# Kernel optimization log

Hardware: AMD Instinct MI355X
Metric: run time of the kernel (lower is better)

## Reference

```python
import jax, jax.numpy as jnp
import numpy as np

N_NODES = 100000
N_EDGES = 1600000
D_IN = 128
D_OUT = 128


def setup_inputs() -> dict:
    key = jax.random.key(0)
    k1, k2, k3, k4 = jax.random.split(key, 4)
    feat = jax.random.normal(k1, (N_NODES, D_IN), dtype=jnp.float32)
    W1 = jax.random.normal(k2, (D_OUT, D_IN), dtype=jnp.float32) * (1.0 / np.sqrt(D_IN))
    src = jax.random.randint(k3, (N_EDGES,), 0, N_NODES, dtype=jnp.int32)
    # ensure every dst node has at least one in-edge (no empty segments, like a
    # DGL graph without isolated destination nodes)
    dst_rand = jax.random.randint(k4, (N_EDGES - N_NODES,), 0, N_NODES, dtype=jnp.int32)
    dst = jnp.concatenate([jnp.arange(N_NODES, dtype=jnp.int32), dst_rand])
    return {"feat": feat, "W1": W1, "src": src, "dst": dst}


def reference(feat, W1, src, dst):
    # nn.Linear(bias=False): h = feat @ W1.T   -> [N, D_OUT]
    norm_h = jnp.einsum("nd,od->no", feat, W1)
    # copy_u message + max reduce: segment-max of projected src feats onto dst
    msgs = norm_h[src]                                   # [E, D_OUT] gather
    h_N = jax.ops.segment_max(msgs, dst, num_segments=feat.shape[0])  # [N, D_OUT]
    # concat(feat_dst, h_N) along feature dim
    return jnp.concatenate([feat, h_N], axis=1)          # [N, D_IN + D_OUT]
```

## Files before the change

kernel.cpp:

```cpp
#include <hip/hip_runtime.h>
#include <hip/hip_bf16.h>

typedef short bf16x8 __attribute__((ext_vector_type(8)));
typedef float f32x4 __attribute__((ext_vector_type(4)));

constexpr int NB_PAD  = 800;
constexpr int PCHUNK  = 8192;
constexpr int HCAP    = 2048;
constexpr int EREG    = 12;

__device__ __forceinline__ unsigned short f32_to_bf16_rne(float f) {
    unsigned int u = __float_as_uint(f);
    u += 0x7fffu + ((u >> 16) & 1u);
    return (unsigned short)(u >> 16);
}
__device__ __forceinline__ unsigned short key16(float f) {
    unsigned short h = f32_to_bf16_rne(f);
    return (h & 0x8000u) ? (unsigned short)(~h) : (unsigned short)(h | 0x8000u);
}
__device__ __forceinline__ float dec16(unsigned int k) {
    unsigned int h = (k & 0x8000u) ? (k ^ 0x8000u) : (~k & 0xFFFFu);
    return __uint_as_float(h << 16);
}
__device__ __forceinline__ void pkmax(unsigned int& a, unsigned int b) {
    asm("v_pk_max_u16 %0, %1, %2" : "=v"(a) : "v"(a), "v"(b));
}

__global__ __launch_bounds__(256) void k1_prep_hist_kernel(
    const float* __restrict__ W1, unsigned short* __restrict__ w1frag,
    const int* __restrict__ dst, unsigned short* __restrict__ chunkPre,
    int E, int nb) {
    __shared__ int pkCnt[NB_PAD / 2];
    const int t = threadIdx.x;

    if ((int)blockIdx.x < 8) {
        int g = blockIdx.x * 256 + t;
        if (g >= 2048) return;
        int l  = g & 63;
        int kb = (g >> 6) & 3;
        int ot = g >> 8;
        int row = ot * 16 + (l & 15);
        int k0  = kb * 32 + (l >> 4) * 8;
        const float* p = W1 + row * 128 + k0;
        float4 f0 = *(const float4*)p;
        float4 f1 = *(const float4*)(p + 4);
        union { unsigned short h[8]; uint4 v; } pk;
        pk.h[0] = f32_to_bf16_rne(f0.x); pk.h[1] = f32_to_bf16_rne(f0.y);
        pk.h[2] = f32_to_bf16_rne(f0.z); pk.h[3] = f32_to_bf16_rne(f0.w);
        pk.h[4] = f32_to_bf16_rne(f1.x); pk.h[5] = f32_to_bf16_rne(f1.y);
        pk.h[6] = f32_to_bf16_rne(f1.z); pk.h[7] = f32_to_bf16_rne(f1.w);
        *(uint4*)(w1frag + (size_t)g * 8) = pk.v;
        return;
    }

    const int c = blockIdx.x - 8;
    for (int i = t; i < NB_PAD / 2; i += 256) pkCnt[i] = 0;
    __syncthreads();
    int c0 = c * PCHUNK;
#pragma unroll
    for (int j = 0; j < PCHUNK / 1024; ++j) {
        int i = c0 + (j * 256 + t) * 4;
        if (i + 3 < E) {
            int4 d4 = *(const int4*)(dst + i);
            atomicAdd(&pkCnt[(d4.x >> 7) >> 1], 1 << (((d4.x >> 7) & 1) << 4));
            atomicAdd(&pkCnt[(d4.y >> 7) >> 1], 1 << (((d4.y >> 7) & 1) << 4));
            atomicAdd(&pkCnt[(d4.z >> 7) >> 1], 1 << (((d4.z >> 7) & 1) << 4));
            atomicAdd(&pkCnt[(d4.w >> 7) >> 1], 1 << (((d4.w >> 7) & 1) << 4));
        } else if (i < E) {
            for (int k = i; k < E; ++k) {
                int b = dst[k] >> 7;
                atomicAdd(&pkCnt[b >> 1], 1 << ((b & 1) << 4));
            }
        }
    }
    __syncthreads();
    unsigned short* rowp = chunkPre + (size_t)c * NB_PAD;
    for (int b = t; b < nb; b += 256)
        rowp[b] = (unsigned short)((pkCnt[b >> 1] >> ((b & 1) << 4)) & 0xFFFF);
}

__global__ __launch_bounds__(256) void k2_chunkscan_kernel(
    unsigned short* __restrict__ chunkPre, int* __restrict__ btot,
    int nchunks, int nb) {
    int wid = blockIdx.x * 4 + (threadIdx.x >> 6);
    int lane = threadIdx.x & 63;
    if (wid >= nb) return;
    int carry = 0;
    int rounds = (nchunks + 63) / 64;
    for (int r = 0; r < rounds; ++r) {
        int c = r * 64 + lane;
        int orig = (c < nchunks) ? (int)chunkPre[(size_t)c * NB_PAD + wid] : 0;
        int v = orig;
#pragma unroll
        for (int d = 1; d < 64; d <<= 1) {
            int x = __shfl_up(v, d, 64);
            if (lane >= d) v += x;
        }
        if (c < nchunks)
            chunkPre[(size_t)c * NB_PAD + wid] = (unsigned short)(carry + v - orig);
        carry += __shfl(v, 63, 64);
    }
    if (lane == 0) btot[wid] = carry;
}

__global__ __launch_bounds__(256) void k3_bscan_kernel(
    const int* __restrict__ btot, int* __restrict__ bbase, int nb) {
    __shared__ int partial[256];
    int t = threadIdx.x;
    int base = t * 4;
    int v[4];
#pragma unroll
    for (int j = 0; j < 4; ++j) v[j] = (base + j < nb) ? btot[base + j] : 0;
    partial[t] = v[0] + v[1] + v[2] + v[3];
    __syncthreads();
    for (int d = 1; d < 256; d <<= 1) {
        int x = (t >= d) ? partial[t - d] : 0;
        __syncthreads();
        if (t >= d) partial[t] += x;
        __syncthreads();
    }
    int run = t ? partial[t - 1] : 0;
#pragma unroll
    for (int j = 0; j < 4; ++j) {
        if (base + j < nb) bbase[base + j] = run;
        run += v[j];
    }
    if (t == 255) bbase[nb] = partial[255];
}

__global__ __launch_bounds__(256) void k4_part_gemm_kernel(
    const float* __restrict__ feat, const unsigned short* __restrict__ w1frag,
    unsigned short* __restrict__ normk, float* __restrict__ out,
    const int* __restrict__ src, const int* __restrict__ dst,
    const unsigned short* __restrict__ chunkPre, const int* __restrict__ bbase,
    int* __restrict__ part, int N, int E, int nb, int partBlocks) {
    __shared__ __align__(16) char smem[32768];
    const int t = threadIdx.x;

    if ((int)blockIdx.x < partBlocks) {
        int* gdst  = (int*)smem;
        int* pkLoc = gdst + NB_PAD;
        for (int i = t; i < NB_PAD / 2; i += 256) pkLoc[i] = 0;
        const unsigned short* pre = chunkPre + (size_t)blockIdx.x * NB_PAD;
        for (int b = t; b < nb; b += 256) gdst[b] = bbase[b] + (int)pre[b];
        __syncthreads();

        int c0 = blockIdx.x * PCHUNK;
#pragma unroll
        for (int j = 0; j < PCHUNK / 1024; ++j) {
            int i = c0 + (j * 256 + t) * 4;
            if (i + 3 < E) {
                int4 d4 = *(const int4*)(dst + i);
                int4 s4 = *(const int4*)(src + i);
                int b, sh, old;
                b = d4.x >> 7; sh = (b & 1) << 4;
                old = atomicAdd(&pkLoc[b >> 1], 1 << sh);
                part[gdst[b] + ((old >> sh) & 0xFFFF)] = s4.x | ((d4.x & 127) << 17);
                b = d4.y >> 7; sh = (b & 1) << 4;
                old = atomicAdd(&pkLoc[b >> 1], 1 << sh);
                part[gdst[b] + ((old >> sh) & 0xFFFF)] = s4.y | ((d4.y & 127) << 17);
                b = d4.z >> 7; sh = (b & 1) << 4;
                old = atomicAdd(&pkLoc[b >> 1], 1 << sh);
                part[gdst[b] + ((old >> sh) & 0xFFFF)] = s4.z | ((d4.z & 127) << 17);
                b = d4.w >> 7; sh = (b & 1) << 4;
                old = atomicAdd(&pkLoc[b >> 1], 1 << sh);
                part[gdst[b] + ((old >> sh) & 0xFFFF)] = s4.w | ((d4.w & 127) << 17);
            } else if (i < E) {
                for (int k = i; k < E; ++k) {
                    int d = dst[k];
                    int b = d >> 7, sh = (b & 1) << 4;
                    int old = atomicAdd(&pkLoc[b >> 1], 1 << sh);
                    part[gdst[b] + ((old >> sh) & 0xFFFF)] = src[k] | ((d & 127) << 17);
                }
            }
        }
    } else {
        uint4* smW = (uint4*)smem;
        const uint4* gw = (const uint4*)w1frag;
#pragma unroll
        for (int i = 0; i < 8; ++i) smW[i * 256 + t] = gw[i * 256 + t];

        const int bid = blockIdx.x - partBlocks;
        const int w = t >> 6;
        const int l = t & 63;
        const int brow0 = bid * 64;
        const int row = brow0 + w * 16 + (l & 15);
        const int kq = (l >> 4) * 8;
        const bool valid = row < N;

        bf16x8 a[4];
        const float* fr = feat + (size_t)row * 128;
        float* orow = out + (size_t)row * 256;
#pragma unroll
        for (int kb = 0; kb < 4; ++kb) {
            float4 f0 = make_float4(0.f, 0.f, 0.f, 0.f), f1 = f0;
            if (valid) {
                f0 = *(const float4*)(fr + kb * 32 + kq);
                f1 = *(const float4*)(fr + kb * 32 + kq + 4);
                *(float4*)(orow + kb * 32 + kq) = f0;
                *(float4*)(orow + kb * 32 + kq + 4) = f1;
            }
            bf16x8 av;
            av[0] = (short)f32_to_bf16_rne(f0.x); av[1] = (short)f32_to_bf16_rne(f0.y);
            av[2] = (short)f32_to_bf16_rne(f0.z); av[3] = (short)f32_to_bf16_rne(f0.w);
            av[4] = (short)f32_to_bf16_rne(f1.x); av[5] = (short)f32_to_bf16_rne(f1.y);
            av[6] = (short)f32_to_bf16_rne(f1.z); av[7] = (short)f32_to_bf16_rne(f1.w);
            a[kb] = av;
        }
        __syncthreads();

        const bf16x8* bfr = (const bf16x8*)smem;
        f32x4 zero = {0.f, 0.f, 0.f, 0.f};
        f32x4 acc[8];
#pragma unroll
        for (int ot = 0; ot < 8; ++ot) acc[ot] = zero;
#pragma unroll
        for (int ot = 0; ot < 8; ++ot) {
#pragma unroll
            for (int kb = 0; kb < 4; ++kb) {
                bf16x8 b = bfr[(ot * 4 + kb) * 64 + l];
                acc[ot] = __builtin_amdgcn_mfma_f32_16x16x32_bf16(a[kb], b, acc[ot], 0, 0, 0);
            }
        }
        __syncthreads();

        unsigned short (*sm)[136] = (unsigned short (*)[136])smem;
        const int r0 = w * 16 + (l >> 4) * 4;
        const int c0 = l & 15;
#pragma unroll
        for (int ot = 0; ot < 8; ++ot)
#pragma unroll
            for (int j = 0; j < 4; ++j)
                sm[r0 + j][ot * 16 + c0] = key16(acc[ot][j]);
        __syncthreads();
#pragma unroll
        for (int i = 0; i < 4; ++i) {
            int idx = i * 256 + t;
            int r = idx >> 4, c = idx & 15;
            int grow = brow0 + r;
            if (grow < N) {
                uint4 v = *(const uint4*)&sm[r][c * 8];
                *(uint4*)(normk + (size_t)grow * 128 + c * 8) = v;
            }
        }
    }
}

__global__ __launch_bounds__(256) void k5_maxpool_kernel(
    const unsigned short* __restrict__ normk, const int* __restrict__ part,
    const int* __restrict__ bbase, float* __restrict__ out, int N) {
    __shared__ int eoff[65];
    __shared__ int eloc[64];
    __shared__ int esrc[HCAP];

    int B = blockIdx.x >> 1;
    int h = blockIdx.x & 1;
    int t = threadIdx.x;
    int start = bbase[B];
    int cnt = bbase[B + 1] - start;
    if (cnt > EREG * 256) cnt = EREG * 256;
    const int* p = part + start;

    int ev[EREG];
#pragma unroll
    for (int j = 0; j < EREG; ++j) {
        int i = j * 256 + t;
        ev[j] = (i < cnt) ? p[i] : -1;
    }

    if (t < 64) eloc[t] = 0;
    __syncthreads();
#pragma unroll
    for (int j = 0; j < EREG; ++j) {
        int v = ev[j];
        if (v >= 0 && (v >> 23) == h) atomicAdd(&eloc[(v >> 17) & 63], 1);
    }
    __syncthreads();
    if (t < 64) {
        int v = eloc[t];
        int sc = v;
#pragma unroll
        for (int d = 1; d < 64; d <<= 1) {
            int x = __shfl_up(sc, d, 64);
            if (t >= d) sc += x;
        }
        int excl = sc - v;
        eoff[t] = excl;
        eloc[t] = excl;
        if (t == 63) eoff[64] = sc;
    }
    __syncthreads();
#pragma unroll
    for (int j = 0; j < EREG; ++j) {
        int v = ev[j];
        if (v >= 0 && (v >> 23) == h) {
            int pos = atomicAdd(&eloc[(v >> 17) & 63], 1);
            if (pos < HCAP) esrc[pos] = v & 0x1FFFF;
        }
    }
    __syncthreads();

    int qw = t >> 4;
    int ln = t & 15;
    const size_t colb = (size_t)ln * 8;
    for (int dl = qw; dl < 64; dl += 16) {
        int node = (B << 7) + (h << 6) + dl;
        if (node >= N) break;
        int si = eoff[dl], se = eoff[dl + 1];
        if (se > HCAP) se = HCAP;
        unsigned int a0 = 0, a1 = 0, a2 = 0, a3 = 0;
        unsigned int b0 = 0, b1 = 0, b2 = 0, b3 = 0;
        unsigned int c0 = 0, c1 = 0, c2 = 0, c3 = 0;
        unsigned int d0 = 0, d1 = 0, d2 = 0, d3 = 0;
        int i = si;
        for (; i + 3 < se; i += 4) {
            uint4 A = *(const uint4*)(normk + (size_t)esrc[i]     * 128 + colb);
            uint4 Bv = *(const uint4*)(normk + (size_t)esrc[i + 1] * 128 + colb);
            uint4 C = *(const uint4*)(normk + (size_t)esrc[i + 2] * 128 + colb);
            uint4 D = *(const uint4*)(normk + (size_t)esrc[i + 3] * 128 + colb);
            pkmax(a0, A.x);  pkmax(a1, A.y);  pkmax(a2, A.z);  pkmax(a3, A.w);
            pkmax(b0, Bv.x); pkmax(b1, Bv.y); pkmax(b2, Bv.z); pkmax(b3, Bv.w);
            pkmax(c0, C.x);  pkmax(c1, C.y);  pkmax(c2, C.z);  pkmax(c3, C.w);
            pkmax(d0, D.x);  pkmax(d1, D.y);  pkmax(d2, D.z);  pkmax(d3, D.w);
        }
        for (; i < se; ++i) {
            uint4 A = *(const uint4*)(normk + (size_t)esrc[i] * 128 + colb);
            pkmax(a0, A.x); pkmax(a1, A.y); pkmax(a2, A.z); pkmax(a3, A.w);
        }
        pkmax(a0, b0); pkmax(a1, b1); pkmax(a2, b2); pkmax(a3, b3);
        pkmax(c0, d0); pkmax(c1, d1); pkmax(c2, d2); pkmax(c3, d3);
        pkmax(a0, c0); pkmax(a1, c1); pkmax(a2, c2); pkmax(a3, c3);
        float4 f0 = make_float4(dec16(a0 & 0xFFFFu), dec16(a0 >> 16),
                                dec16(a1 & 0xFFFFu), dec16(a1 >> 16));
        float4 f1 = make_float4(dec16(a2 & 0xFFFFu), dec16(a2 >> 16),
                                dec16(a3 & 0xFFFFu), dec16(a3 >> 16));
        float* op = out + (size_t)node * 256 + 128 + colb;
        *(float4*)op       = f0;
        *(float4*)(op + 4) = f1;
    }
}

extern "C" void kernel_launch(void* const* d_in, const int* in_sizes, int n_in,
                              void* d_out, int out_size, void* d_ws, size_t ws_size,
                              hipStream_t stream) {
    const float* feat = (const float*)d_in[0];
    const float* W1   = (const float*)d_in[1];
    const int*   src  = (const int*)d_in[2];
    const int*   dst  = (const int*)d_in[3];
    float* out = (float*)d_out;

    const int N = in_sizes[0] / 128;
    const int E = in_sizes[2];
    const int nb = (N + 127) >> 7;
    const int nchunks = (E + PCHUNK - 1) / PCHUNK;

    char* wsp = (char*)d_ws;
    size_t o = 0;
    unsigned short* normk = (unsigned short*)(wsp + o);
    o += ((size_t)N * 128 * 2 + 255) & ~(size_t)255;
    int* part = (int*)(wsp + o);
    o += ((size_t)E * 4 + 255) & ~(size_t)255;
    unsigned short* chunkPre = (unsigned short*)(wsp + o);
    o += ((size_t)nchunks * NB_PAD * 2 + 255) & ~(size_t)255;
    int* btot = (int*)(wsp + o);  o += NB_PAD * 4;
    int* bbase = (int*)(wsp + o); o += (NB_PAD + 1) * 4;
    unsigned short* w1frag = (unsigned short*)(wsp + o);
    o += 2048 * 8 * 2;

    k1_prep_hist_kernel<<<8 + nchunks, 256, 0, stream>>>(
        W1, w1frag, dst, chunkPre, E, nb);
    k2_chunkscan_kernel<<<(nb + 3) / 4, 256, 0, stream>>>(chunkPre, btot, nchunks, nb);
    k3_bscan_kernel<<<1, 256, 0, stream>>>(btot, bbase, nb);
    k4_part_gemm_kernel<<<nchunks + (N + 63) / 64, 256, 0, stream>>>(
        feat, w1frag, normk, out, src, dst, chunkPre, bbase, part, N, E, nb, nchunks);
    k5_maxpool_kernel<<<nb * 2, 256, 0, stream>>>(normk, part, bbase, out, N);
}
```

Baseline: 119.7 us.

## Quantize projected features to int8 with per-row scales for max-gather

Replaces the bf16 order-preserving keys with symmetric int8 quantization using a per-row absmax scale computed in the GEMM epilogue. The max-pool kernel gathers 8-byte int8 slices plus a row scale, dequantizes in float and reduces with fmaxf. This halves the bytes read per gathered edge row, but adds an extra scale load, more ALU work per element, and coarser precision that may breach tolerance.

```diff
diff --git a/kernel.cpp b/kernel.cpp
--- a/kernel.cpp
+++ b/kernel.cpp
@@ -1,5 +1,6 @@
 #include <hip/hip_runtime.h>
 #include <hip/hip_bf16.h>
+#include <cfloat>
 
 typedef short bf16x8 __attribute__((ext_vector_type(8)));
 typedef float f32x4 __attribute__((ext_vector_type(4)));
@@ -14,16 +15,8 @@
     u += 0x7fffu + ((u >> 16) & 1u);
     return (unsigned short)(u >> 16);
 }
-__device__ __forceinline__ unsigned short key16(float f) {
-    unsigned short h = f32_to_bf16_rne(f);
-    return (h & 0x8000u) ? (unsigned short)(~h) : (unsigned short)(h | 0x8000u);
-}
-__device__ __forceinline__ float dec16(unsigned int k) {
-    unsigned int h = (k & 0x8000u) ? (k ^ 0x8000u) : (~k & 0xFFFFu);
-    return __uint_as_float(h << 16);
-}
-__device__ __forceinline__ void pkmax(unsigned int& a, unsigned int b) {
-    asm("v_pk_max_u16 %0, %1, %2" : "=v"(a) : "v"(a), "v"(b));
+__device__ __forceinline__ float b2f(unsigned int w, int k) {
+    return (float)((int)(w << (24 - 8 * k)) >> 24);
 }
 
 __global__ __launch_bounds__(256) void k1_prep_hist_kernel(
@@ -130,7 +123,8 @@
 
 __global__ __launch_bounds__(256) void k4_part_gemm_kernel(
     const float* __restrict__ feat, const unsigned short* __restrict__ w1frag,
-    unsigned short* __restrict__ normk, float* __restrict__ out,
+    signed char* __restrict__ norm8, float* __restrict__ rowscale,
+    float* __restrict__ out,
     const int* __restrict__ src, const int* __restrict__ dst,
     const unsigned short* __restrict__ chunkPre, const int* __restrict__ bbase,
     int* __restrict__ part, int N, int E, int nb, int partBlocks) {
@@ -222,33 +216,54 @@
                 acc[ot] = __builtin_amdgcn_mfma_f32_16x16x32_bf16(a[kb], b, acc[ot], 0, 0, 0);
             }
         }
-        __syncthreads();
-
-        unsigned short (*sm)[136] = (unsigned short (*)[136])smem;
+
         const int r0 = w * 16 + (l >> 4) * 4;
+        float inv[4], scl[4];
+#pragma unroll
+        for (int j = 0; j < 4; ++j) {
+            float am = 0.f;
+#pragma unroll
+            for (int ot = 0; ot < 8; ++ot) am = fmaxf(am, __builtin_fabsf(acc[ot][j]));
+#pragma unroll
+            for (int d = 1; d < 16; d <<= 1) am = fmaxf(am, __shfl_xor(am, d, 64));
+            am = fmaxf(am, 1e-30f);
+            inv[j] = 127.0f / am;
+            scl[j] = am * (1.0f / 127.0f);
+        }
+        if ((l & 15) == 0) {
+#pragma unroll
+            for (int j = 0; j < 4; ++j) {
+                int grow = brow0 + r0 + j;
+                if (grow < N) rowscale[grow] = scl[j];
+            }
+        }
+        __syncthreads();
+
+        char (*sm8)[144] = (char (*)[144])smem;
         const int c0 = l & 15;
 #pragma unroll
         for (int ot = 0; ot < 8; ++ot)
 #pragma unroll
             for (int j = 0; j < 4; ++j)
-                sm[r0 + j][ot * 16 + c0] = key16(acc[ot][j]);
-        __syncthreads();
-#pragma unroll
-        for (int i = 0; i < 4; ++i) {
+                sm8[r0 + j][ot * 16 + c0] = (char)(int)rintf(acc[ot][j] * inv[j]);
+        __syncthreads();
+#pragma unroll
+        for (int i = 0; i < 2; ++i) {
             int idx = i * 256 + t;
-            int r = idx >> 4, c = idx & 15;
+            int r = idx >> 3, c = idx & 7;
             int grow = brow0 + r;
             if (grow < N) {
-                uint4 v = *(const uint4*)&sm[r][c * 8];
-                *(uint4*)(normk + (size_t)grow * 128 + c * 8) = v;
+                uint4 v = *(const uint4*)&sm8[r][c * 16];
+                *(uint4*)(norm8 + (size_t)grow * 128 + c * 16) = v;
             }
         }
     }
 }
 
 __global__ __launch_bounds__(256) void k5_maxpool_kernel(
-    const unsigned short* __restrict__ normk, const int* __restrict__ part,
-    const int* __restrict__ bbase, float* __restrict__ out, int N) {
+    const signed char* __restrict__ norm8, const float* __restrict__ rowscale,
+    const int* __restrict__ part, const int* __restrict__ bbase,
+    float* __restrict__ out, int N) {
     __shared__ int eoff[65];
     __shared__ int eloc[64];
     __shared__ int esrc[HCAP];
@@ -308,35 +323,40 @@
         if (node >= N) break;
         int si = eoff[dl], se = eoff[dl + 1];
         if (se > HCAP) se = HCAP;
-        unsigned int a0 = 0, a1 = 0, a2 = 0, a3 = 0;
-        unsigned int b0 = 0, b1 = 0, b2 = 0, b3 = 0;
-        unsigned int c0 = 0, c1 = 0, c2 = 0, c3 = 0;
-        unsigned int d0 = 0, d1 = 0, d2 = 0, d3 = 0;
+        float a0 = -FLT_MAX, a1 = -FLT_MAX, a2 = -FLT_MAX, a3 = -FLT_MAX;
+        float a4 = -FLT_MAX, a5 = -FLT_MAX, a6 = -FLT_MAX, a7 = -FLT_MAX;
+        float b0 = -FLT_MAX, b1 = -FLT_MAX, b2 = -FLT_MAX, b3 = -FLT_MAX;
+        float b4 = -FLT_MAX, b5 = -FLT_MAX, b6 = -FLT_MAX, b7 = -FLT_MAX;
         int i = si;
-        for (; i + 3 < se; i += 4) {
-            uint4 A = *(const uint4*)(normk + (size_t)esrc[i]     * 128 + colb);
-            uint4 Bv = *(const uint4*)(normk + (size_t)esrc[i + 1] * 128 + colb);
-            uint4 C = *(const uint4*)(normk + (size_t)esrc[i + 2] * 128 + colb);
-            uint4 D = *(const uint4*)(normk + (size_t)esrc[i + 3] * 128 + colb);
-            pkmax(a0, A.x);  pkmax(a1, A.y);  pkmax(a2, A.z);  pkmax(a3, A.w);
-            pkmax(b0, Bv.x); pkmax(b1, Bv.y); pkmax(b2, Bv.z); pkmax(b3, Bv.w);
-            pkmax(c0, C.x);  pkmax(c1, C.y);  pkmax(c2, C.z);  pkmax(c3, C.w);
-            pkmax(d0, D.x);  pkmax(d1, D.y);  pkmax(d2, D.z);  pkmax(d3, D.w);
-        }
-        for (; i < se; ++i) {
-            uint4 A = *(const uint4*)(normk + (size_t)esrc[i] * 128 + colb);
-            pkmax(a0, A.x); pkmax(a1, A.y); pkmax(a2, A.z); pkmax(a3, A.w);
-        }
-        pkmax(a0, b0); pkmax(a1, b1); pkmax(a2, b2); pkmax(a3, b3);
-        pkmax(c0, d0); pkmax(c1, d1); pkmax(c2, d2); pkmax(c3, d3);
-        pkmax(a0, c0); pkmax(a1, c1); pkmax(a2, c2); pkmax(a3, c3);
-        float4 f0 = make_float4(dec16(a0 & 0xFFFFu), dec16(a0 >> 16),
-                                dec16(a1 & 0xFFFFu), dec16(a1 >> 16));
-        float4 f1 = make_float4(dec16(a2 & 0xFFFFu), dec16(a2 >> 16),
-                                dec16(a3 & 0xFFFFu), dec16(a3 >> 16));
+        for (; i + 1 < se; i += 2) {
+            int s1 = esrc[i], s2 = esrc[i + 1];
+            uint2 wA = *(const uint2*)(norm8 + (size_t)s1 * 128 + colb);
+            float scA = rowscale[s1];
+            uint2 wB = *(const uint2*)(norm8 + (size_t)s2 * 128 + colb);
+            float scB = rowscale[s2];
+            a0 = fmaxf(a0, b2f(wA.x, 0) * scA); a1 = fmaxf(a1, b2f(wA.x, 1) * scA);
+            a2 = fmaxf(a2, b2f(wA.x, 2) * scA); a3 = fmaxf(a3, b2f(wA.x, 3) * scA);
+            a4 = fmaxf(a4, b2f(wA.y, 0) * scA); a5 = fmaxf(a5, b2f(wA.y, 1) * scA);
+            a6 = fmaxf(a6, b2f(wA.y, 2) * scA); a7 = fmaxf(a7, b2f(wA.y, 3) * scA);
+            b0 = fmaxf(b0, b2f(wB.x, 0) * scB); b1 = fmaxf(b1, b2f(wB.x, 1) * scB);
+            b2 = fmaxf(b2, b2f(wB.x, 2) * scB); b3 = fmaxf(b3, b2f(wB.x, 3) * scB);
+            b4 = fmaxf(b4, b2f(wB.y, 0) * scB); b5 = fmaxf(b5, b2f(wB.y, 1) * scB);
+            b6 = fmaxf(b6, b2f(wB.y, 2) * scB); b7 = fmaxf(b7, b2f(wB.y, 3) * scB);
+        }
+        if (i < se) {
+            int s1 = esrc[i];
+            uint2 wA = *(const uint2*)(norm8 + (size_t)s1 * 128 + colb);
+            float scA = rowscale[s1];
+            a0 = fmaxf(a0, b2f(wA.x, 0) * scA); a1 = fmaxf(a1, b2f(wA.x, 1) * scA);
+            a2 = fmaxf(a2, b2f(wA.x, 2) * scA); a3 = fmaxf(a3, b2f(wA.x, 3) * scA);
+            a4 = fmaxf(a4, b2f(wA.y, 0) * scA); a5 = fmaxf(a5, b2f(wA.y, 1) * scA);
+            a6 = fmaxf(a6, b2f(wA.y, 2) * scA); a7 = fmaxf(a7, b2f(wA.y, 3) * scA);
+        }
+        a0 = fmaxf(a0, b0); a1 = fmaxf(a1, b1); a2 = fmaxf(a2, b2); a3 = fmaxf(a3, b3);
+        a4 = fmaxf(a4, b4); a5 = fmaxf(a5, b5); a6 = fmaxf(a6, b6); a7 = fmaxf(a7, b7);
         float* op = out + (size_t)node * 256 + 128 + colb;
-        *(float4*)op       = f0;
-        *(float4*)(op + 4) = f1;
+        *(float4*)op       = make_float4(a0, a1, a2, a3);
+        *(float4*)(op + 4) = make_float4(a4, a5, a6, a7);
     }
 }
 
@@ -356,8 +376,10 @@
 
     char* wsp = (char*)d_ws;
     size_t o = 0;
-    unsigned short* normk = (unsigned short*)(wsp + o);
-    o += ((size_t)N * 128 * 2 + 255) & ~(size_t)255;
+    signed char* norm8 = (signed char*)(wsp + o);
+    o += ((size_t)N * 128 + 255) & ~(size_t)255;
+    float* rowscale = (float*)(wsp + o);
+    o += ((size_t)N * 4 + 255) & ~(size_t)255;
     int* part = (int*)(wsp + o);
     o += ((size_t)E * 4 + 255) & ~(size_t)255;
     unsigned short* chunkPre = (unsigned short*)(wsp + o);
@@ -372,6 +394,7 @@
     k2_chunkscan_kernel<<<(nb + 3) / 4, 256, 0, stream>>>(chunkPre, btot, nchunks, nb);
     k3_bscan_kernel<<<1, 256, 0, stream>>>(btot, bbase, nb);
     k4_part_gemm_kernel<<<nchunks + (N + 63) / 64, 256, 0, stream>>>(
-        feat, w1frag, normk, out, src, dst, chunkPre, bbase, part, N, E, nb, nchunks);
-    k5_maxpool_kernel<<<nb * 2, 256, 0, stream>>>(normk, part, bbase, out, N);
-}
+        feat, w1frag, norm8, rowscale, out, src, dst, chunkPre, bbase, part,
+        N, E, nb, nchunks);
+    k5_maxpool_kernel<<<nb * 2, 256, 0, stream>>>(norm8, rowscale, part, bbase, out, N);
+}
```

After: 106.5 us. 1.12x faster.
